# Kernel tuning notes

Hardware: AMD Instinct MI355X
Metric: run time of the kernel (lower is better)

## Reference

```python
import jax, jax.numpy as jnp
import numpy as np

C, S, K, SIGMA = 512, 11, 3, 16
B = 128
EPS = 1e-5  # BatchNorm eps (eval mode, running_mean=0, running_var=1)


def _make_dct_weight(Cc, H, W):
    # FcaNet 'low16' frequency selection
    lx = [0, 0, 1, 1, 0, 2, 2, 1, 2, 0, 3, 4, 0, 1, 3, 0]
    ly = [0, 1, 0, 1, 2, 0, 1, 2, 2, 3, 0, 0, 4, 3, 1, 5]
    mx = [u * (H // 7) for u in lx]
    my = [v * (W // 7) for v in ly]
    w = np.zeros((Cc, H, W), np.float32)
    cp = Cc // len(lx)

    def bf(pos, freq, POS):
        r = np.cos(np.pi * freq * (pos + 0.5) / POS) / np.sqrt(POS)
        return r if freq == 0 else r * np.sqrt(2.0)

    for i, (u, v) in enumerate(zip(mx, my)):
        for tx in range(H):
            for ty in range(W):
                w[i * cp:(i + 1) * cp, tx, ty] = bf(tx, u, H) * bf(ty, v, W)
    return jnp.asarray(w)


def _bn(f, g, b):
    # eval-mode BatchNorm2d: (f - 0)/sqrt(1+eps)*g + b, per channel (axis 1)
    s = g / jnp.sqrt(1.0 + EPS)
    return f * s[None, :, None, None] + b[None, :, None, None]


def _conv1x1(f, w, b):
    return jnp.einsum('bchw,oc->bohw', f, w) + b[None, :, None, None]


def _spatial_kernel(f, w_conv, b_conv, g_sp, b_sp):
    Bn = f.shape[0]
    s = _conv1x1(f, w_conv, b_conv)                  # (B, K*K, S, S)
    s = s.reshape(Bn, K * K, S * S).transpose(0, 2, 1)  # (B, S*S, K*K)
    s = _bn(s.reshape(Bn, S * S, K, K), g_sp, b_sp)
    return s.reshape(Bn, S * S, K * K)


def _channel_kernel(f, dct_w, fc1, fc2, g_ch, b_ch):
    y = jnp.sum(f * dct_w[None], axis=(-2, -1))      # (B, C) DCT pooling
    y = jax.nn.sigmoid(jax.nn.relu(y @ fc1.T) @ fc2.T)  # (B, C*K*K)
    y = _bn(y.reshape(-1, C, K, K), g_ch, b_ch)
    return y.reshape(-1, C, K * K)


def _unfold(f):
    # torch-style per-pixel kxk neighborhoods -> (B, C, H, W, K, K)
    p = (K + 1) // 2 - 1
    Bn, Cn, H, W = f.shape
    fp = jnp.pad(f, ((0, 0), (0, 0), (p, p), (p, p)))
    pat = jnp.stack([fp[:, :, di:di + H, dj:dj + W]
                     for di in range(K) for dj in range(K)], axis=-1)
    return pat.reshape(Bn, Cn, H, W, K, K)


def setup_inputs() -> dict:
    key = jax.random.key(0)
    ks = iter(jax.random.split(key, 32))

    def nrm(shape, s=0.02):
        return s * jax.random.normal(next(ks), shape, jnp.float32)

    def gma(shape):
        return 1.0 + 0.1 * jax.random.normal(next(ks), shape, jnp.float32)

    return dict(
        x=jax.random.normal(next(ks), (B, C, S, S), jnp.float32),
        dct_w=_make_dct_weight(C, S, S),
        w_conv=nrm((K * K, C)), b_conv=nrm((K * K,)),
        g_sp=gma((S * S,)), b_sp=nrm((S * S,), 0.05),
        g_ch=gma((C,)), b_ch=nrm((C,), 0.05),
        fc1=nrm((C // SIGMA, C)), fc2=nrm((C * K * K, C // SIGMA)),
        up_w1=nrm((2 * C, C)), up_b1=nrm((2 * C,)), up_g1=gma((2 * C,)), up_bb1=nrm((2 * C,), 0.05),
        up_w2=nrm((2 * C, 2 * C)), up_b2=nrm((2 * C,)), up_g2=gma((2 * C,)), up_bb2=nrm((2 * C,), 0.05),
        lo_w1=nrm((2 * C, 2 * C)), lo_b1=nrm((2 * C,)), lo_g1=gma((2 * C,)), lo_bb1=nrm((2 * C,), 0.05),
        lo_w2=nrm((C, 2 * C)), lo_b2=nrm((C,)), lo_g2=gma((C,)), lo_bb2=nrm((C,), 0.05),
    )


def reference(x, dct_w, w_conv, b_conv, g_sp, b_sp, g_ch, b_ch, fc1, fc2,
              up_w1, up_b1, up_g1, up_bb1, up_w2, up_b2, up_g2, up_bb2,
              lo_w1, lo_b1, lo_g1, lo_bb1, lo_w2, lo_b2, lo_g2, lo_bb2):
    Bn = x.shape[0]
    # instance kernel: spatial (B,1,HW,KK) x channel (B,C,1,KK)
    sk = _spatial_kernel(x, w_conv, b_conv, g_sp, b_sp)[:, None]
    ck = _channel_kernel(x, dct_w, fc1, fc2, g_ch, b_ch)[:, :, None]
    inst = (sk * ck).reshape(Bn, C, S, S, K, K)
    # CLM task representation (sum over batch between upper and lower)
    a = jax.nn.relu(_bn(_conv1x1(x, up_w1, up_b1), up_g1, up_bb1))
    a = jax.nn.relu(_bn(_conv1x1(a, up_w2, up_b2), up_g2, up_bb2))
    a = a.sum(axis=0, keepdims=True)
    a = jax.nn.relu(_bn(_conv1x1(a, lo_w1, lo_b1), lo_g1, lo_bb1))
    task_s = jax.nn.sigmoid(_bn(_conv1x1(a, lo_w2, lo_b2), lo_g2, lo_bb2))
    # task kernel (shared across the batch)
    sk_t = _spatial_kernel(task_s, w_conv, b_conv, g_sp, b_sp)[:, None]
    ck_t = _channel_kernel(task_s, dct_w, fc1, fc2, g_ch, b_ch)[:, :, None]
    task_kernel = (sk_t * ck_t).reshape(1, C, S, S, K, K)
    kernel = task_kernel * inst
    adapted = (_unfold(x) * kernel).mean(axis=(-1, -2))  # (B,C,S,S)
    return adapted + x, task_kernel
```

## Files before the change

### kernel.cpp

```cpp
#include <hip/hip_runtime.h>
#include <hip/hip_bf16.h>
#include <math.h>

#define BNEPS 1e-5f
#define BDIM_B 128
#define CDIM 512
#define SS 121
#define KK 9
#define MROWS (BDIM_B * SS)

typedef unsigned short u16;
typedef __bf16 bf16x8 __attribute__((ext_vector_type(8)));
typedef float f32x4 __attribute__((ext_vector_type(4)));

__device__ __forceinline__ u16 f2bf(float f) {
    union { float f; unsigned int u; } v; v.f = f;
    unsigned int r = v.u + 0x7FFF + ((v.u >> 16) & 1);
    return (u16)(r >> 16);
}
__device__ __forceinline__ float bf2f(u16 v) {
    union { unsigned int u; float f; } x; x.u = ((unsigned int)v) << 16; return x.f;
}

__device__ __forceinline__ void gld16(const u16* g, u16* l) {
    __builtin_amdgcn_global_load_lds(
        (const __attribute__((address_space(1))) void*)g,
        (__attribute__((address_space(3))) void*)l, 16, 0, 0);
}

template<int MODE>
__device__ __forceinline__ void gemm128_body(
    const u16* __restrict__ A, const u16* __restrict__ Bw,
    const float* __restrict__ bias, const float* __restrict__ g,
    const float* __restrict__ bb, void* __restrict__ out,
    int Kd, int N, int bi)
{
    __shared__ __align__(16) u16 Als[2][128 * 32];
    __shared__ __align__(16) u16 Bls[2][128 * 32];

    const int tid  = threadIdx.x;
    const int lane = tid & 63;
    const int w    = tid >> 6;
    const int wm   = w >> 1, wn = w & 1;

    int bx, by;
    {
        int i = bi;
        if (i < 960) {
            int xg = i & 7;
            int j  = i >> 3;
            bx = xg * 15 + (j >> 3);
            by = j & 7;
        } else { bx = 120; by = i - 960; }
    }
    const int bm = bx * 128;
    const int bn = by * 128;

    f32x4 acc[4][4] = {};

    const int subrow = tid >> 2;
    const int kq     = tid & 3;
    const int gchunk = kq ^ ((subrow >> 1) & 3);
    const u16* Ab = A  + (size_t)(bm + subrow) * Kd + gchunk * 8;
    const u16* Bb = Bw + (size_t)(bn + subrow) * Kd + gchunk * 8;
    u16* Al0  = &Als[0][(w * 16) * 32];
    u16* Al1  = &Als[0][(w * 16 + 64) * 32];
    u16* Bl0  = &Bls[0][(w * 16) * 32];
    u16* Bl1  = &Bls[0][(w * 16 + 64) * 32];
    u16* Al0b = &Als[1][(w * 16) * 32];
    u16* Al1b = &Als[1][(w * 16 + 64) * 32];
    u16* Bl0b = &Bls[1][(w * 16) * 32];
    u16* Bl1b = &Bls[1][(w * 16 + 64) * 32];

    const int fa_row = wm * 64 + (lane & 15);
    const int fb_row = wn * 64 + (lane & 15);
    const int kofs   = (((lane >> 4) ^ (((lane & 15) >> 1) & 3))) * 8;

    for (int k0 = 0; k0 < Kd; k0 += 64) {
        __syncthreads();
        gld16(Ab + k0,                      Al0);
        gld16(Ab + (size_t)64 * Kd + k0,    Al1);
        gld16(Bb + k0,                      Bl0);
        gld16(Bb + (size_t)64 * Kd + k0,    Bl1);
        gld16(Ab + k0 + 32,                 Al0b);
        gld16(Ab + (size_t)64 * Kd + k0 + 32, Al1b);
        gld16(Bb + k0 + 32,                 Bl0b);
        gld16(Bb + (size_t)64 * Kd + k0 + 32, Bl1b);
        __syncthreads();

        #pragma unroll
        for (int hb = 0; hb < 2; ++hb) {
            const u16* Ah = &Als[hb][0];
            const u16* Bh = &Bls[hb][0];
            bf16x8 af[4], bfv[4];
            #pragma unroll
            for (int i = 0; i < 4; ++i)
                af[i] = *(const bf16x8*)&Ah[(fa_row + i * 16) * 32 + kofs];
            #pragma unroll
            for (int j = 0; j < 4; ++j)
                bfv[j] = *(const bf16x8*)&Bh[(fb_row + j * 16) * 32 + kofs];
            #pragma unroll
            for (int i = 0; i < 4; ++i)
                #pragma unroll
                for (int j = 0; j < 4; ++j)
                    acc[i][j] = __builtin_amdgcn_mfma_f32_16x16x32_bf16(af[i], bfv[j], acc[i][j], 0, 0, 0);
        }
    }

    const float inv = 1.0f / sqrtf(1.0f + BNEPS);

    if (MODE == 1) {
        u16* Y = (u16*)out;
        int dstrow[4][4];
        #pragma unroll
        for (int i = 0; i < 4; ++i) {
            int mb = bm + wm * 64 + i * 16 + (lane >> 4) * 4;
            #pragma unroll
            for (int r = 0; r < 4; ++r) {
                int m = mb + r;
                int b = m / 121, p = m - b * 121;
                dstrow[i][r] = p * 128 + b;
            }
        }
        #pragma unroll
        for (int j = 0; j < 4; ++j) {
            int n = bn + wn * 64 + j * 16 + (lane & 15);
            float sc = g[n] * inv, bo = bias[n], bv = bb[n];
            #pragma unroll
            for (int i = 0; i < 4; ++i)
                #pragma unroll
                for (int r = 0; r < 4; ++r) {
                    float v = (acc[i][j][r] + bo) * sc + bv;
                    v = fmaxf(v, 0.0f);
                    Y[(size_t)dstrow[i][r] * N + n] = f2bf(v);
                }
        }
    } else {
        float ps[4];
        #pragma unroll
        for (int j = 0; j < 4; ++j) {
            int n = bn + wn * 64 + j * 16 + (lane & 15);
            float sc = g[n] * inv, bo = bias[n], bv = bb[n];
            float s = 0.f;
            #pragma unroll
            for (int i = 0; i < 4; ++i)
                #pragma unroll
                for (int r = 0; r < 4; ++r) {
                    float v = (acc[i][j][r] + bo) * sc + bv;
                    s += fmaxf(v, 0.0f);
                }
            ps[j] = s;
        }
        __syncthreads();
        float* red = (float*)Als;
        #pragma unroll
        for (int j = 0; j < 4; ++j)
            red[(wm * 4 + (lane >> 4)) * 128 + wn * 64 + j * 16 + (lane & 15)] = ps[j];
        __syncthreads();
        if (tid < 128) {
            float s = 0.f;
            #pragma unroll
            for (int r = 0; r < 8; ++r) s += red[r * 128 + tid];
            ((u16*)out)[(size_t)bx * N + bn + tid] = f2bf(s);
        }
    }
}

template<int MODE>
__device__ __forceinline__ void gemm_small_body(
    const u16* __restrict__ A, const u16* __restrict__ Bw,
    const float* __restrict__ bias, const float* __restrict__ g,
    const float* __restrict__ bb, u16* __restrict__ Y,
    int Kd, int N, int bn)
{
    const int tid  = threadIdx.x;
    const int lane = tid & 63;
    const int w    = tid >> 6;
    const int fr   = lane & 15;
    const int kq   = lane >> 4;
    const int r0   = w * 32;

    f32x4 acc[2][4] = {};
    const u16* a0p = A + (size_t)(r0 + fr) * Kd + kq * 8;
    const u16* a1p = a0p + (size_t)16 * Kd;
    const u16* bp  = Bw + (size_t)(bn + fr) * Kd + kq * 8;

    #pragma unroll 4
    for (int k0 = 0; k0 < Kd; k0 += 32) {
        bf16x8 a0 = *(const bf16x8*)(a0p + k0);
        bf16x8 a1 = *(const bf16x8*)(a1p + k0);
        #pragma unroll
        for (int j = 0; j < 4; ++j) {
            bf16x8 bv = *(const bf16x8*)(bp + (size_t)j * 16 * Kd + k0);
            acc[0][j] = __builtin_amdgcn_mfma_f32_16x16x32_bf16(a0, bv, acc[0][j], 0, 0, 0);
            acc[1][j] = __builtin_amdgcn_mfma_f32_16x16x32_bf16(a1, bv, acc[1][j], 0, 0, 0);
        }
    }

    const float inv = 1.0f / sqrtf(1.0f + BNEPS);
    #pragma unroll
    for (int j = 0; j < 4; ++j) {
        int n = bn + j * 16 + (lane & 15);
        float sc = g[n] * inv, bo = bias[n], bv = bb[n];
        #pragma unroll
        for (int t = 0; t < 2; ++t)
            #pragma unroll
            for (int r = 0; r < 4; ++r) {
                int m = r0 + t * 16 + (lane >> 4) * 4 + r;
                float v = (acc[t][j][r] + bo) * sc + bv;
                if (MODE == 3) v = fmaxf(v, 0.0f);
                else           v = 1.f / (1.f + expf(-v));
                Y[(size_t)m * N + n] = f2bf(v);
            }
    }
}

__device__ __forceinline__ void spatial_body(
    const u16* __restrict__ Arow, const u16* __restrict__ wcb,
    const float* __restrict__ b_conv, const float* __restrict__ g_sp,
    const float* __restrict__ b_sp, float* __restrict__ skb,
    bool task, int blk, float* __restrict__ skt)
{
    const float inv = 1.0f / sqrtf(1.0f + BNEPS);
    const int lane = threadIdx.x & 63;
    const int w    = threadIdx.x >> 6;
    const int fr   = lane & 15;
    const int kq   = lane >> 4;
    const int r0   = w * 32;

    f32x4 acc0 = {}, acc1 = {};
    const u16* a0p = Arow + (size_t)(r0 + fr) * 512 + kq * 8;
    const u16* a1p = a0p + (size_t)16 * 512;
    const u16* bp  = wcb + (size_t)fr * 512 + kq * 8;
    #pragma unroll
    for (int k0 = 0; k0 < 512; k0 += 32) {
        bf16x8 a0 = *(const bf16x8*)(a0p + k0);
        bf16x8 a1 = *(const bf16x8*)(a1p + k0);
        bf16x8 b  = *(const bf16x8*)(bp + k0);
        acc0 = __builtin_amdgcn_mfma_f32_16x16x32_bf16(a0, b, acc0, 0, 0, 0);
        acc1 = __builtin_amdgcn_mfma_f32_16x16x32_bf16(a1, b, acc1, 0, 0, 0);
    }

    int n = lane & 15;
    if (n < 9) {
        float bo = b_conv[n];
        #pragma unroll
        for (int t = 0; t < 2; ++t) {
            f32x4 a = t ? acc1 : acc0;
            #pragma unroll
            for (int r = 0; r < 4; ++r) {
                int mloc = r0 + t * 16 + (lane >> 4) * 4 + r;
                if (!task) {
                    int m = blk * 128 + mloc;
                    int p = m % 121;
                    float v = (a[r] + bo) * (g_sp[p] * inv) + b_sp[p];
                    skb[(size_t)m * 9 + n] = v;
                } else if (mloc < 121) {
                    float v = (a[r] + bo) * (g_sp[mloc] * inv) + b_sp[mloc];
                    skt[(size_t)mloc * 9 + n] = v;
                }
            }
        }
    }
}

__device__ __forceinline__ void channel_body(
    const u16* __restrict__ src, const float* __restrict__ dctT,
    const float* __restrict__ fc1, const float* __restrict__ fc2,
    const float* __restrict__ g_ch, const float* __restrict__ b_ch,
    float* __restrict__ outp, float* yls, float* y2ls)
{
    const float inv = 1.0f / sqrtf(1.0f + BNEPS);

    {
        int c = threadIdx.x * 2;
        float s0 = 0.f, s1 = 0.f;
        for (int p = 0; p < SS; ++p) {
            unsigned v = *(const unsigned*)(src + (size_t)p * 512 + c);
            float2 d  = *(const float2*)(dctT + (size_t)p * 512 + c);
            s0 += bf2f((u16)(v & 0xFFFFu)) * d.x;
            s1 += bf2f((u16)(v >> 16)) * d.y;
        }
        yls[c] = s0; yls[c + 1] = s1;
    }
    __syncthreads();

    {
        int o = threadIdx.x >> 3, kp = threadIdx.x & 7;
        const float* w = fc1 + (size_t)o * 512;
        float s = 0.f;
        for (int k = kp * 4; k < 512; k += 32) {
            float4 wv = *(const float4*)(w + k);
            float4 av = *(const float4*)(yls + k);
            s += wv.x * av.x + wv.y * av.y + wv.z * av.z + wv.w * av.w;
        }
        s += __shfl_xor(s, 1);
        s += __shfl_xor(s, 2);
        s += __shfl_xor(s, 4);
        if (kp == 0) y2ls[o] = fmaxf(s, 0.f);
    }
    __syncthreads();

    for (int o = threadIdx.x; o < CDIM * KK; o += 256) {
        const float* w = fc2 + (size_t)o * 32;
        float s = 0.f;
        #pragma unroll
        for (int k = 0; k < 32; ++k) s += y2ls[k] * w[k];
        s = 1.f / (1.f + expf(-s));
        int c = o / KK;
        s = s * (g_ch[c] * inv) + b_ch[c];
        outp[o] = s;
    }
}

template<int MODE>
__global__ __launch_bounds__(256)
void gemm_mfma(const u16* __restrict__ A, const u16* __restrict__ Bw,
               const float* __restrict__ bias, const float* __restrict__ g,
               const float* __restrict__ bb, void* __restrict__ out,
               int Kd, int N)
{
    gemm128_body<MODE>(A, Bw, bias, g, bb, out, Kd, N, blockIdx.x);
}

__global__ __launch_bounds__(256)
void mega1(const u16* __restrict__ Xb, const u16* __restrict__ w1b,
           const float* __restrict__ up_b1, const float* __restrict__ up_g1,
           const float* __restrict__ up_bb1, u16* __restrict__ Y1,
           const u16* __restrict__ wcb, const float* __restrict__ b_conv,
           const float* __restrict__ g_sp, const float* __restrict__ b_sp,
           const float* __restrict__ dctT,
           const float* __restrict__ fc1, const float* __restrict__ fc2,
           const float* __restrict__ g_ch, const float* __restrict__ b_ch,
           float* __restrict__ skb, float* __restrict__ ckbuf)
{
    __shared__ float sm[544];
    int bi = blockIdx.x;
    if (bi < 968) {
        gemm128_body<1>(Xb, w1b, up_b1, up_g1, up_bb1, (void*)Y1, 512, 1024, bi);
        return;
    }
    bi -= 968;
    if (bi < 121) {
        spatial_body(Xb + (size_t)bi * 128 * 512, wcb, b_conv, g_sp, b_sp,
                     skb, false, bi, nullptr);
        return;
    }
    bi -= 121;
    channel_body(Xb + (size_t)bi * 121 * 512, dctT, fc1, fc2, g_ch, b_ch,
                 ckbuf + (size_t)bi * CDIM * KK, sm, sm + 512);
}

__device__ __forceinline__ void gbar(int* bar, int target)
{
    __syncthreads();
    if (threadIdx.x == 0) {
        __threadfence();
        atomicAdd(bar, 1);
        while (atomicAdd(bar, 0) < target) { }
        __threadfence();
    }
    __syncthreads();
}

__global__ __launch_bounds__(256)
void lo_chain(const u16* __restrict__ asum_b, const u16* __restrict__ lw1b,
              const float* __restrict__ lo_b1, const float* __restrict__ lo_g1,
              const float* __restrict__ lo_bb1, u16* __restrict__ a3b,
              const u16* __restrict__ lw2b,
              const float* __restrict__ lo_b2, const float* __restrict__ lo_g2,
              const float* __restrict__ lo_bb2, u16* __restrict__ ts_pc,
              const u16* __restrict__ wcb, const float* __restrict__ b_conv,
              const float* __restrict__ g_sp, const float* __restrict__ b_sp,
              const float* __restrict__ dctT,
              const float* __restrict__ fc1, const float* __restrict__ fc2,
              const float* __restrict__ g_ch, const float* __restrict__ b_ch,
              float* __restrict__ skt, float* __restrict__ ck_t,
              int* __restrict__ bar)
{
    __shared__ float sm[544];

    gemm_small_body<3>(asum_b, lw1b, lo_b1, lo_g1, lo_bb1, a3b, 1024, 1024,
                       blockIdx.x * 64);
    gbar(bar, 16);

    if (blockIdx.x < 8)
        gemm_small_body<4>(a3b, lw2b, lo_b2, lo_g2, lo_bb2, ts_pc, 1024, 512,
                           blockIdx.x * 64);
    gbar(bar, 32);

    if (blockIdx.x == 0)
        spatial_body(ts_pc, wcb, b_conv, g_sp, b_sp, nullptr, true, 0, skt);
    else if (blockIdx.x == 1)
        channel_body(ts_pc, dctT, fc1, fc2, g_ch, b_ch, ck_t, sm, sm + 512);
}

#define W1N (1024 * 512)
#define W2N (1024 * 1024)
#define L1N (1024 * 1024)
#define L2N (512 * 1024)
#define VECN ((W1N + W2N + L1N + L2N) / 4)
#define DCTN (512 * 121)
#define WCN (16 * 512)
#define PREP_ELEM (VECN + DCTN + WCN)
#define PREP_BLKS (1024 + (PREP_ELEM + 255) / 256)
__global__ void prep_combo(const float* __restrict__ x, u16* __restrict__ Xb,
                           const float* __restrict__ w1, const float* __restrict__ w2,
                           const float* __restrict__ l1, const float* __restrict__ l2,
                           const float* __restrict__ dct, const float* __restrict__ w_conv,
                           u16* __restrict__ o1, u16* __restrict__ o2,
                           u16* __restrict__ o3, u16* __restrict__ o4,
                           float* __restrict__ dctT, u16* __restrict__ wcb,
                           int* __restrict__ bar)
{
    __shared__ float t[64 * 121];
    if (blockIdx.x == 0 && threadIdx.x == 0) *bar = 0;
    if (blockIdx.x < 1024) {
        int b = blockIdx.x >> 3, c0 = (blockIdx.x & 7) * 64;
        for (int idx = threadIdx.x; idx < 64 * 121; idx += 256) {
            int c = idx / 121, p = idx - c * 121;
            t[idx] = x[((size_t)b * 512 + c0 + c) * 121 + p];
        }
        __syncthreads();
        for (int idx = threadIdx.x; idx < 121 * 64; idx += 256) {
            int p = idx >> 6, c = idx & 63;
            Xb[((size_t)(b * 121 + p)) * 512 + c0 + c] = f2bf(t[c * 121 + p]);
        }
        return;
    }
    int i = (blockIdx.x - 1024) * 256 + threadIdx.x;
    if (i < VECN) {
        int q = i;
        const float* s; u16* d;
        if (q < W1N / 4)                    { s = w1; d = o1; }
        else if (q < (W1N + W2N) / 4)       { s = w2; d = o2; q -= W1N / 4; }
        else if (q < (W1N + W2N + L1N) / 4) { s = l1; d = o3; q -= (W1N + W2N) / 4; }
        else                                { s = l2; d = o4; q -= (W1N + W2N + L1N) / 4; }
        float4 v = ((const float4*)s)[q];
        uint2 r;
        r.x = (unsigned)f2bf(v.x) | ((unsigned)f2bf(v.y) << 16);
        r.y = (unsigned)f2bf(v.z) | ((unsigned)f2bf(v.w) << 16);
        ((uint2*)d)[q] = r;
        return;
    }
    i -= VECN;
    if (i < DCTN) {
        int p = i >> 9, c = i & 511;
        dctT[i] = dct[(size_t)c * 121 + p];
        return;
    }
    i -= DCTN;
    if (i < WCN) {
        int n = i >> 9, c = i & 511;
        wcb[i] = (n < 9) ? f2bf(w_conv[(size_t)n * 512 + c]) : (u16)0;
    }
}

#define TKN (CDIM * SS * KK)
#define FIN_BLKS (1024 + (TKN + 255) / 256)
__global__ __launch_bounds__(256)
void final_combo(const float* __restrict__ x, const float* __restrict__ skb,
                 const float* __restrict__ sk_t, const float* __restrict__ ckbuf,
                 const float* __restrict__ ck_t, float* __restrict__ out0,
                 float* __restrict__ tk)
{
    __shared__ float PS[SS * KK];
    __shared__ float CS[64 * KK];
    __shared__ float XT[64 * SS];

    if (blockIdx.x >= 1024) {
        int idx = (blockIdx.x - 1024) * 256 + threadIdx.x;
        if (idx < TKN) {
            int k9 = idx % KK;
            int pc = idx / KK;
            int p = pc % SS, c = pc / SS;
            tk[idx] = sk_t[p * KK + k9] * ck_t[c * KK + k9];
        }
        return;
    }

    const int tid = threadIdx.x;
    const int b = blockIdx.x >> 3, c0 = (blockIdx.x & 7) * 64;

    const float* sp = skb + (size_t)b * SS * KK;
    for (int i = tid; i < SS * KK; i += 256) PS[i] = sp[i] * sk_t[i];
    const float* cp = ckbuf + ((size_t)b * CDIM + c0) * KK;
    const float* tp = ck_t + (size_t)c0 * KK;
    for (int i = tid; i < (64 * KK) / 4; i += 256) {
        float4 a = ((const float4*)cp)[i];
        float4 bq = ((const float4*)tp)[i];
        float4 r; r.x = a.x * bq.x; r.y = a.y * bq.y; r.z = a.z * bq.z; r.w = a.w * bq.w;
        ((float4*)CS)[i] = r;
    }
    const float* xp = x + ((size_t)b * CDIM + c0) * SS;
    for (int i = tid; i < (64 * SS) / 4; i += 256)
        ((float4*)XT)[i] = ((const float4*)xp)[i];
    __syncthreads();

    float* op = out0 + ((size_t)b * CDIM + c0) * SS;
    for (int ci = tid; ci < (64 * SS) / 4; ci += 256) {
        float4 o;
        #pragma unroll
        for (int r = 0; r < 4; ++r) {
            int i = ci * 4 + r;
            int c = i / SS, p = i - c * SS;
            int h = p / 11, w = p - h * 11;
            const float* xc = XT + c * SS;
            const float* ps = PS + p * KK;
            const float* cs = CS + c * KK;
            float acc = 0.f;
            #pragma unroll
            for (int di = 0; di < 3; ++di) {
                int hh = h + di - 1;
                bool hv = (unsigned)hh < 11u;
                #pragma unroll
                for (int dj = 0; dj < 3; ++dj) {
                    int ww = w + dj - 1;
                    int k = di * 3 + dj;
                    float xv = (hv && (unsigned)ww < 11u) ? xc[hh * 11 + ww] : 0.f;
                    acc += xv * ps[k] * cs[k];
                }
            }
            ((float*)&o)[r] = acc * (1.0f / 9.0f) + xc[p];
        }
        ((float4*)op)[ci] = o;
    }
}

extern "C" void kernel_launch(void* const* d_in, const int* in_sizes, int n_in,
                              void* d_out, int out_size, void* d_ws, size_t ws_size,
                              hipStream_t stream)
{
    const float* x      = (const float*)d_in[0];
    const float* dct_w  = (const float*)d_in[1];
    const float* w_conv = (const float*)d_in[2];
    const float* b_conv = (const float*)d_in[3];
    const float* g_sp   = (const float*)d_in[4];
    const float* b_sp   = (const float*)d_in[5];
    const float* g_ch   = (const float*)d_in[6];
    const float* b_ch   = (const float*)d_in[7];
    const float* fc1    = (const float*)d_in[8];
    const float* fc2    = (const float*)d_in[9];
    const float* up_w1  = (const float*)d_in[10];
    const float* up_b1  = (const float*)d_in[11];
    const float* up_g1  = (const float*)d_in[12];
    const float* up_bb1 = (const float*)d_in[13];
    const float* up_w2  = (const float*)d_in[14];
    const float* up_b2  = (const float*)d_in[15];
    const float* up_g2  = (const float*)d_in[16];
    const float* up_bb2 = (const float*)d_in[17];
    const float* lo_w1  = (const float*)d_in[18];
    const float* lo_b1  = (const float*)d_in[19];
    const float* lo_g1  = (const float*)d_in[20];
    const float* lo_bb1 = (const float*)d_in[21];
    const float* lo_w2  = (const float*)d_in[22];
    const float* lo_b2  = (const float*)d_in[23];
    const float* lo_g2  = (const float*)d_in[24];
    const float* lo_bb2 = (const float*)d_in[25];

    float* out0 = (float*)d_out;
    float* tk   = out0 + (size_t)BDIM_B * CDIM * SS;

    char* ws = (char*)d_ws;
    size_t off = 0;
    auto alloc = [&](size_t bytes) { void* p = ws + off; off += (bytes + 63) & ~(size_t)63; return p; };
    u16*   Xb      = (u16*)alloc((size_t)MROWS * 512 * 2);
    u16*   Y1      = (u16*)alloc((size_t)MROWS * 1024 * 2);
    u16*   w1b     = (u16*)alloc((size_t)W1N * 2);
    u16*   w2b     = (u16*)alloc((size_t)W2N * 2);
    u16*   lw1b    = (u16*)alloc((size_t)L1N * 2);
    u16*   lw2b    = (u16*)alloc((size_t)L2N * 2);
    u16*   asum_b  = (u16*)alloc((size_t)128 * 1024 * 2);
    u16*   a3b     = (u16*)alloc((size_t)128 * 1024 * 2);
    u16*   ts_pc   = (u16*)alloc((size_t)128 * 512 * 2);
    float* dctT    = (float*)alloc((size_t)SS * 512 * 4);
    u16*   wcb     = (u16*)alloc((size_t)WCN * 2);
    float* ckbuf   = (float*)alloc((size_t)BDIM_B * CDIM * KK * 4);
    float* skbuf   = (float*)alloc((size_t)BDIM_B * SS * KK * 4);
    float* ck_t    = (float*)alloc((size_t)CDIM * KK * 4);
    float* sk_t    = (float*)alloc((size_t)SS * KK * 4);
    int*   bar     = (int*)alloc(64);

    hipLaunchKernelGGL(prep_combo, dim3(PREP_BLKS), dim3(256), 0, stream,
                       x, Xb, up_w1, up_w2, lo_w1, lo_w2, dct_w, w_conv,
                       w1b, w2b, lw1b, lw2b, dctT, wcb, bar);

    hipLaunchKernelGGL(mega1, dim3(968 + 121 + 128), dim3(256), 0, stream,
                       Xb, w1b, up_b1, up_g1, up_bb1, Y1,
                       wcb, b_conv, g_sp, b_sp,
                       dctT, fc1, fc2, g_ch, b_ch,
                       skbuf, ckbuf);

    hipLaunchKernelGGL((gemm_mfma<2>), dim3(121 * 8), dim3(256), 0, stream,
                       Y1, w2b, up_b2, up_g2, up_bb2, (void*)asum_b, 1024, 1024);

    hipLaunchKernelGGL(lo_chain, dim3(16), dim3(256), 0, stream,
                       asum_b, lw1b, lo_b1, lo_g1, lo_bb1, a3b,
                       lw2b, lo_b2, lo_g2, lo_bb2, ts_pc,
                       wcb, b_conv, g_sp, b_sp,
                       dctT, fc1, fc2, g_ch, b_ch,
                       sk_t, ck_t, bar);

    hipLaunchKernelGGL(final_combo, dim3(FIN_BLKS), dim3(256), 0, stream,
                       x, skbuf, sk_t, ckbuf, ck_t, out0, tk);
}
```

Baseline: 380.4 us.

## Fuse layer-2 GEMM and lo chain into one cooperative kernel with grid syncs

Merges the second up-projection GEMM, the two small lo-branch GEMMs and the task-kernel computation into a single cooperative launch separated by grid.sync, replacing a separate kernel plus a 16-block chain with a hand-rolled atomic barrier. The small GEMMs now use 32-column tiles spread over more blocks (32 and 16 instead of 16 and 8) to widen parallelism on the serial tail. Shared memory is passed in explicitly so the fused kernels can reuse one buffer. The cooperative launch requires all 968 blocks to be co-resident; if the launch fails, the code falls back to four separate launches.

```diff
diff --git a/kernel.cpp b/kernel.cpp
--- a/kernel.cpp
+++ b/kernel.cpp
@@ -1,6 +1,9 @@
 #include <hip/hip_runtime.h>
 #include <hip/hip_bf16.h>
+#include <hip/hip_cooperative_groups.h>
 #include <math.h>
+
+namespace cg = cooperative_groups;
 
 #define BNEPS 1e-5f
 #define BDIM_B 128
@@ -33,11 +36,8 @@
     const u16* __restrict__ A, const u16* __restrict__ Bw,
     const float* __restrict__ bias, const float* __restrict__ g,
     const float* __restrict__ bb, void* __restrict__ out,
-    int Kd, int N, int bi)
-{
-    __shared__ __align__(16) u16 Als[2][128 * 32];
-    __shared__ __align__(16) u16 Bls[2][128 * 32];
-
+    int Kd, int N, int bi, u16* AlsB, u16* BlsB)
+{
     const int tid  = threadIdx.x;
     const int lane = tid & 63;
     const int w    = tid >> 6;
@@ -63,14 +63,14 @@
     const int gchunk = kq ^ ((subrow >> 1) & 3);
     const u16* Ab = A  + (size_t)(bm + subrow) * Kd + gchunk * 8;
     const u16* Bb = Bw + (size_t)(bn + subrow) * Kd + gchunk * 8;
-    u16* Al0  = &Als[0][(w * 16) * 32];
-    u16* Al1  = &Als[0][(w * 16 + 64) * 32];
-    u16* Bl0  = &Bls[0][(w * 16) * 32];
-    u16* Bl1  = &Bls[0][(w * 16 + 64) * 32];
-    u16* Al0b = &Als[1][(w * 16) * 32];
-    u16* Al1b = &Als[1][(w * 16 + 64) * 32];
-    u16* Bl0b = &Bls[1][(w * 16) * 32];
-    u16* Bl1b = &Bls[1][(w * 16 + 64) * 32];
+    u16* Al0  = AlsB + (w * 16) * 32;
+    u16* Al1  = AlsB + (w * 16 + 64) * 32;
+    u16* Bl0  = BlsB + (w * 16) * 32;
+    u16* Bl1  = BlsB + (w * 16 + 64) * 32;
+    u16* Al0b = AlsB + 4096 + (w * 16) * 32;
+    u16* Al1b = AlsB + 4096 + (w * 16 + 64) * 32;
+    u16* Bl0b = BlsB + 4096 + (w * 16) * 32;
+    u16* Bl1b = BlsB + 4096 + (w * 16 + 64) * 32;
 
     const int fa_row = wm * 64 + (lane & 15);
     const int fb_row = wn * 64 + (lane & 15);
@@ -90,8 +90,8 @@
 
         #pragma unroll
         for (int hb = 0; hb < 2; ++hb) {
-            const u16* Ah = &Als[hb][0];
-            const u16* Bh = &Bls[hb][0];
+            const u16* Ah = AlsB + hb * 4096;
+            const u16* Bh = BlsB + hb * 4096;
             bf16x8 af[4], bfv[4];
             #pragma unroll
             for (int i = 0; i < 4; ++i)
@@ -152,7 +152,7 @@
             ps[j] = s;
         }
         __syncthreads();
-        float* red = (float*)Als;
+        float* red = (float*)AlsB;
         #pragma unroll
         for (int j = 0; j < 4; ++j)
             red[(wm * 4 + (lane >> 4)) * 128 + wn * 64 + j * 16 + (lane & 15)] = ps[j];
@@ -180,26 +180,27 @@
     const int kq   = lane >> 4;
     const int r0   = w * 32;
 
-    f32x4 acc[2][4] = {};
+    f32x4 acc[2][2] = {};
     const u16* a0p = A + (size_t)(r0 + fr) * Kd + kq * 8;
     const u16* a1p = a0p + (size_t)16 * Kd;
-    const u16* bp  = Bw + (size_t)(bn + fr) * Kd + kq * 8;
+    const u16* b0p = Bw + (size_t)(bn + fr) * Kd + kq * 8;
+    const u16* b1p = b0p + (size_t)16 * Kd;
 
     #pragma unroll 4
     for (int k0 = 0; k0 < Kd; k0 += 32) {
         bf16x8 a0 = *(const bf16x8*)(a0p + k0);
         bf16x8 a1 = *(const bf16x8*)(a1p + k0);
-        #pragma unroll
-        for (int j = 0; j < 4; ++j) {
-            bf16x8 bv = *(const bf16x8*)(bp + (size_t)j * 16 * Kd + k0);
-            acc[0][j] = __builtin_amdgcn_mfma_f32_16x16x32_bf16(a0, bv, acc[0][j], 0, 0, 0);
-            acc[1][j] = __builtin_amdgcn_mfma_f32_16x16x32_bf16(a1, bv, acc[1][j], 0, 0, 0);
-        }
+        bf16x8 b0 = *(const bf16x8*)(b0p + k0);
+        bf16x8 b1 = *(const bf16x8*)(b1p + k0);
+        acc[0][0] = __builtin_amdgcn_mfma_f32_16x16x32_bf16(a0, b0, acc[0][0], 0, 0, 0);
+        acc[0][1] = __builtin_amdgcn_mfma_f32_16x16x32_bf16(a0, b1, acc[0][1], 0, 0, 0);
+        acc[1][0] = __builtin_amdgcn_mfma_f32_16x16x32_bf16(a1, b0, acc[1][0], 0, 0, 0);
+        acc[1][1] = __builtin_amdgcn_mfma_f32_16x16x32_bf16(a1, b1, acc[1][1], 0, 0, 0);
     }
 
     const float inv = 1.0f / sqrtf(1.0f + BNEPS);
     #pragma unroll
-    for (int j = 0; j < 4; ++j) {
+    for (int j = 0; j < 2; ++j) {
         int n = bn + j * 16 + (lane & 15);
         float sc = g[n] * inv, bo = bias[n], bv = bb[n];
         #pragma unroll
@@ -313,16 +314,6 @@
     }
 }
 
-template<int MODE>
-__global__ __launch_bounds__(256)
-void gemm_mfma(const u16* __restrict__ A, const u16* __restrict__ Bw,
-               const float* __restrict__ bias, const float* __restrict__ g,
-               const float* __restrict__ bb, void* __restrict__ out,
-               int Kd, int N)
-{
-    gemm128_body<MODE>(A, Bw, bias, g, bb, out, Kd, N, blockIdx.x);
-}
-
 __global__ __launch_bounds__(256)
 void mega1(const u16* __restrict__ Xb, const u16* __restrict__ w1b,
            const float* __restrict__ up_b1, const float* __restrict__ up_g1,
@@ -334,10 +325,11 @@
            const float* __restrict__ g_ch, const float* __restrict__ b_ch,
            float* __restrict__ skb, float* __restrict__ ckbuf)
 {
-    __shared__ float sm[544];
+    __shared__ __align__(16) u16 shmem[4][128 * 32];
     int bi = blockIdx.x;
     if (bi < 968) {
-        gemm128_body<1>(Xb, w1b, up_b1, up_g1, up_bb1, (void*)Y1, 512, 1024, bi);
+        gemm128_body<1>(Xb, w1b, up_b1, up_g1, up_bb1, (void*)Y1, 512, 1024, bi,
+                        &shmem[0][0], &shmem[2][0]);
         return;
     }
     bi -= 968;
@@ -347,51 +339,90 @@
         return;
     }
     bi -= 121;
+    float* sm = (float*)&shmem[0][0];
     channel_body(Xb + (size_t)bi * 121 * 512, dctT, fc1, fc2, g_ch, b_ch,
                  ckbuf + (size_t)bi * CDIM * KK, sm, sm + 512);
 }
 
-__device__ __forceinline__ void gbar(int* bar, int target)
-{
-    __syncthreads();
-    if (threadIdx.x == 0) {
-        __threadfence();
-        atomicAdd(bar, 1);
-        while (atomicAdd(bar, 0) < target) { }
-        __threadfence();
-    }
-    __syncthreads();
-}
-
+__global__ __launch_bounds__(256, 4)
+void coop_chain(const u16* __restrict__ Y1, const u16* __restrict__ w2b,
+                const float* __restrict__ up_b2, const float* __restrict__ up_g2,
+                const float* __restrict__ up_bb2, u16* __restrict__ asum_b,
+                const u16* __restrict__ lw1b,
+                const float* __restrict__ lo_b1, const float* __restrict__ lo_g1,
+                const float* __restrict__ lo_bb1, u16* __restrict__ a3b,
+                const u16* __restrict__ lw2b,
+                const float* __restrict__ lo_b2, const float* __restrict__ lo_g2,
+                const float* __restrict__ lo_bb2, u16* __restrict__ ts_pc,
+                const u16* __restrict__ wcb, const float* __restrict__ b_conv,
+                const float* __restrict__ g_sp, const float* __restrict__ b_sp,
+                const float* __restrict__ dctT,
+                const float* __restrict__ fc1, const float* __restrict__ fc2,
+                const float* __restrict__ g_ch, const float* __restrict__ b_ch,
+                float* __restrict__ skt, float* __restrict__ ck_t)
+{
+    __shared__ __align__(16) u16 shmem[4][128 * 32];
+    cg::grid_group grid = cg::this_grid();
+
+    gemm128_body<2>(Y1, w2b, up_b2, up_g2, up_bb2, (void*)asum_b, 1024, 1024,
+                    blockIdx.x, &shmem[0][0], &shmem[2][0]);
+    __threadfence();
+    grid.sync();
+
+    if (blockIdx.x < 32)
+        gemm_small_body<3>(asum_b, lw1b, lo_b1, lo_g1, lo_bb1, a3b, 1024, 1024,
+                           blockIdx.x * 32);
+    __threadfence();
+    grid.sync();
+
+    if (blockIdx.x < 16)
+        gemm_small_body<4>(a3b, lw2b, lo_b2, lo_g2, lo_bb2, ts_pc, 1024, 512,
+                           blockIdx.x * 32);
+    __threadfence();
+    grid.sync();
+
+    if (blockIdx.x == 0) {
+        spatial_body(ts_pc, wcb, b_conv, g_sp, b_sp, nullptr, true, 0, skt);
+    } else if (blockIdx.x == 1) {
+        float* sm = (float*)&shmem[0][0];
+        channel_body(ts_pc, dctT, fc1, fc2, g_ch, b_ch, ck_t, sm, sm + 512);
+    }
+}
+
+template<int MODE>
 __global__ __launch_bounds__(256)
-void lo_chain(const u16* __restrict__ asum_b, const u16* __restrict__ lw1b,
-              const float* __restrict__ lo_b1, const float* __restrict__ lo_g1,
-              const float* __restrict__ lo_bb1, u16* __restrict__ a3b,
-              const u16* __restrict__ lw2b,
-              const float* __restrict__ lo_b2, const float* __restrict__ lo_g2,
-              const float* __restrict__ lo_bb2, u16* __restrict__ ts_pc,
-              const u16* __restrict__ wcb, const float* __restrict__ b_conv,
-              const float* __restrict__ g_sp, const float* __restrict__ b_sp,
-              const float* __restrict__ dctT,
-              const float* __restrict__ fc1, const float* __restrict__ fc2,
-              const float* __restrict__ g_ch, const float* __restrict__ b_ch,
-              float* __restrict__ skt, float* __restrict__ ck_t,
-              int* __restrict__ bar)
+void gemm_mfma(const u16* __restrict__ A, const u16* __restrict__ Bw,
+               const float* __restrict__ bias, const float* __restrict__ g,
+               const float* __restrict__ bb, void* __restrict__ out,
+               int Kd, int N)
+{
+    __shared__ __align__(16) u16 shmem[4][128 * 32];
+    gemm128_body<MODE>(A, Bw, bias, g, bb, out, Kd, N, blockIdx.x,
+                       &shmem[0][0], &shmem[2][0]);
+}
+
+template<int MODE>
+__global__ __launch_bounds__(256)
+void gemm_small(const u16* __restrict__ A, const u16* __restrict__ Bw,
+                const float* __restrict__ bias, const float* __restrict__ g,
+                const float* __restrict__ bb, u16* __restrict__ Y,
+                int Kd, int N)
+{
+    gemm_small_body<MODE>(A, Bw, bias, g, bb, Y, Kd, N, blockIdx.x * 32);
+}
+
+__global__ __launch_bounds__(256)
+void task_combo(const u16* __restrict__ ts_pc, const u16* __restrict__ wcb,
+                const float* __restrict__ b_conv, const float* __restrict__ g_sp,
+                const float* __restrict__ b_sp, const float* __restrict__ dctT,
+                const float* __restrict__ fc1, const float* __restrict__ fc2,
+                const float* __restrict__ g_ch, const float* __restrict__ b_ch,
+                float* __restrict__ skt, float* __restrict__ ck_t)
 {
     __shared__ float sm[544];
-
-    gemm_small_body<3>(asum_b, lw1b, lo_b1, lo_g1, lo_bb1, a3b, 1024, 1024,
-                       blockIdx.x * 64);
-    gbar(bar, 16);
-
-    if (blockIdx.x < 8)
-        gemm_small_body<4>(a3b, lw2b, lo_b2, lo_g2, lo_bb2, ts_pc, 1024, 512,
-                           blockIdx.x * 64);
-    gbar(bar, 32);
-
     if (blockIdx.x == 0)
         spatial_body(ts_pc, wcb, b_conv, g_sp, b_sp, nullptr, true, 0, skt);
-    else if (blockIdx.x == 1)
+    else
         channel_body(ts_pc, dctT, fc1, fc2, g_ch, b_ch, ck_t, sm, sm + 512);
 }
 
@@ -410,11 +441,9 @@
                            const float* __restrict__ dct, const float* __restrict__ w_conv,
                            u16* __restrict__ o1, u16* __restrict__ o2,
                            u16* __restrict__ o3, u16* __restrict__ o4,
-                           float* __restrict__ dctT, u16* __restrict__ wcb,
-                           int* __restrict__ bar)
+                           float* __restrict__ dctT, u16* __restrict__ wcb)
 {
     __shared__ float t[64 * 121];
-    if (blockIdx.x == 0 && threadIdx.x == 0) *bar = 0;
     if (blockIdx.x < 1024) {
         int b = blockIdx.x >> 3, c0 = (blockIdx.x & 7) * 64;
         for (int idx = threadIdx.x; idx < 64 * 121; idx += 256) {
@@ -579,11 +608,10 @@
     float* skbuf   = (float*)alloc((size_t)BDIM_B * SS * KK * 4);
     float* ck_t    = (float*)alloc((size_t)CDIM * KK * 4);
     float* sk_t    = (float*)alloc((size_t)SS * KK * 4);
-    int*   bar     = (int*)alloc(64);
 
     hipLaunchKernelGGL(prep_combo, dim3(PREP_BLKS), dim3(256), 0, stream,
                        x, Xb, up_w1, up_w2, lo_w1, lo_w2, dct_w, w_conv,
-                       w1b, w2b, lw1b, lw2b, dctT, wcb, bar);
+                       w1b, w2b, lw1b, lw2b, dctT, wcb);
 
     hipLaunchKernelGGL(mega1, dim3(968 + 121 + 128), dim3(256), 0, stream,
                        Xb, w1b, up_b1, up_g1, up_bb1, Y1,
@@ -591,15 +619,46 @@
                        dctT, fc1, fc2, g_ch, b_ch,
                        skbuf, ckbuf);
 
-    hipLaunchKernelGGL((gemm_mfma<2>), dim3(121 * 8), dim3(256), 0, stream,
-                       Y1, w2b, up_b2, up_g2, up_bb2, (void*)asum_b, 1024, 1024);
-
-    hipLaunchKernelGGL(lo_chain, dim3(16), dim3(256), 0, stream,
-                       asum_b, lw1b, lo_b1, lo_g1, lo_bb1, a3b,
-                       lw2b, lo_b2, lo_g2, lo_bb2, ts_pc,
-                       wcb, b_conv, g_sp, b_sp,
-                       dctT, fc1, fc2, g_ch, b_ch,
-                       sk_t, ck_t, bar);
+    {
+        const u16* aY1 = Y1;       const u16* aw2b = w2b;
+        const float* ab2 = up_b2;  const float* ag2 = up_g2;  const float* abb2 = up_bb2;
+        u16* aasum = asum_b;
+        const u16* alw1 = lw1b;
+        const float* alb1 = lo_b1; const float* alg1 = lo_g1; const float* albb1 = lo_bb1;
+        u16* aa3 = a3b;
+        const u16* alw2 = lw2b;
+        const float* alb2 = lo_b2; const float* alg2 = lo_g2; const float* albb2 = lo_bb2;
+        u16* ats = ts_pc;
+        const u16* awcb = wcb;     const float* abconv = b_conv;
+        const float* agsp = g_sp;  const float* absp = b_sp;
+        const float* adctT = dctT; const float* afc1 = fc1;   const float* afc2 = fc2;
+        const float* agch = g_ch;  const float* abch = b_ch;
+        float* askt = sk_t;        float* ackt = ck_t;
+
+        void* coopArgs[] = {
+            (void*)&aY1, (void*)&aw2b, (void*)&ab2, (void*)&ag2, (void*)&abb2,
+            (void*)&aasum,
+            (void*)&alw1, (void*)&alb1, (void*)&alg1, (void*)&albb1, (void*)&aa3,
+            (void*)&alw2, (void*)&alb2, (void*)&alg2, (void*)&albb2, (void*)&ats,
+            (void*)&awcb, (void*)&abconv, (void*)&agsp, (void*)&absp,
+            (void*)&adctT, (void*)&afc1, (void*)&afc2, (void*)&agch, (void*)&abch,
+            (void*)&askt, (void*)&ackt
+        };
+        hipError_t e = hipLaunchCooperativeKernel(
+            reinterpret_cast<void*>(&coop_chain), dim3(968), dim3(256),
+            coopArgs, 0, stream);
+        if (e != hipSuccess) {
+            hipLaunchKernelGGL((gemm_mfma<2>), dim3(968), dim3(256), 0, stream,
+                               Y1, w2b, up_b2, up_g2, up_bb2, (void*)asum_b, 1024, 1024);
+            hipLaunchKernelGGL((gemm_small<3>), dim3(32), dim3(256), 0, stream,
+                               asum_b, lw1b, lo_b1, lo_g1, lo_bb1, a3b, 1024, 1024);
+            hipLaunchKernelGGL((gemm_small<4>), dim3(16), dim3(256), 0, stream,
+                               a3b, lw2b, lo_b2, lo_g2, lo_bb2, ts_pc, 1024, 512);
+            hipLaunchKernelGGL(task_combo, dim3(2), dim3(256), 0, stream,
+                               ts_pc, wcb, b_conv, g_sp, b_sp,
+                               dctT, fc1, fc2, g_ch, b_ch, sk_t, ck_t);
+        }
+    }
 
     hipLaunchKernelGGL(final_combo, dim3(FIN_BLKS), dim3(256), 0, stream,
                        x, skbuf, sk_t, ckbuf, ck_t, out0, tk);
```

Result: slower. 927.7 us (+143.8%).
